# Performance work log

Hardware: AMD Instinct MI355X
Metric: run time of the kernel (lower is better)

## Reference

```python
import jax, jax.numpy as jnp
import numpy as np

N = 50000      # nodes
IN = 256       # in_feat
H = 4          # num_heads
DH = 64        # out_feat // num_heads
R = 6          # number of relations
E = 300000     # edges per relation
NEG_SLOPE = 0.2  # DGL GATConv leaky_relu slope


def setup_inputs() -> dict:
    key = jax.random.key(0)
    ks = jax.random.split(key, 7)
    x = jax.random.normal(ks[0], (N, IN), dtype=jnp.float32)
    W = jax.random.normal(ks[1], (R, IN, H * DH), dtype=jnp.float32) * (1.0 / np.sqrt(IN))
    attn_l = jax.random.normal(ks[2], (R, H, DH), dtype=jnp.float32) * 0.1
    attn_r = jax.random.normal(ks[3], (R, H, DH), dtype=jnp.float32) * 0.1
    bias = jax.random.normal(ks[4], (R, H * DH), dtype=jnp.float32) * 0.01
    src = jax.random.randint(ks[5], (R, E), 0, N, dtype=jnp.int32).astype(jnp.int64)
    dst = jax.random.randint(ks[6], (R, E), 0, N, dtype=jnp.int32).astype(jnp.int64)
    return {"x": x, "W": W, "attn_l": attn_l, "attn_r": attn_r, "bias": bias,
            "src": src, "dst": dst}


def reference(x, W, attn_l, attn_r, bias, src, dst):
    n = x.shape[0]
    r_total, h, dh = attn_l.shape
    out = jnp.zeros((n, h, dh), dtype=x.dtype)
    # small fixed loop over structurally-distinct relations (HeteroGraphConv)
    for r in range(r_total):
        feat = (x @ W[r]).reshape(n, h, dh)            # [N,H,Dh] shared src/dst proj
        el = jnp.sum(feat * attn_l[r], axis=-1)        # [N,H]
        er = jnp.sum(feat * attn_r[r], axis=-1)        # [N,H]
        s, d = src[r], dst[r]
        e = jax.nn.leaky_relu(el[s] + er[d], NEG_SLOPE)  # [E,H]
        # segmented softmax over incoming edges of each dst node
        m = jax.ops.segment_max(e, d, num_segments=n)    # [N,H]
        m = jnp.where(jnp.isfinite(m), m, 0.0)
        a = jnp.exp(e - m[d])                            # [E,H]
        z = jax.ops.segment_sum(a, d, num_segments=n)    # [N,H]
        alpha = a / jnp.maximum(z[d], 1e-9)              # [E,H]
        msg = alpha[:, :, None] * feat[s]                # [E,H,Dh]
        agg = jax.ops.segment_sum(msg, d, num_segments=n)  # [N,H,Dh]
        # GATConv: bias + activation(relu) per relation, HeteroGraphConv sums
        out = out + jax.nn.relu(agg + bias[r].reshape(h, dh))
    hcat = out.reshape(n, h * dh)                        # merge='cat' view
    return jax.nn.relu(hcat)                             # layer-level activation
```

## Files before the change

kernel.cpp:

```cpp
#include <hip/hip_runtime.h>

#define NN 50000
#define MP 50048
#define NH 4
#define NR 6
#define NE 300000
#define HD 256
#define SLOTS 32
#define NB 512
#define BSZ ((NE + NB - 1) / NB)

typedef __attribute__((ext_vector_type(4))) float f32x4;
typedef __attribute__((ext_vector_type(8))) short bf16x8;

__device__ __forceinline__ short f2bf(float f) {
  unsigned u = __float_as_uint(f);
  unsigned r = (u + 0x7FFFu + ((u >> 16) & 1u)) >> 16;
  return (short)r;
}
__device__ __forceinline__ float bf2f_lo(unsigned d) {
  return __uint_as_float(d << 16);
}
__device__ __forceinline__ float bf2f_hi(unsigned d) {
  return __uint_as_float(d & 0xffff0000u);
}

#define GLOAD_LDS16(g, l)                                                     \
  __builtin_amdgcn_global_load_lds(                                           \
      (const __attribute__((address_space(1))) void*)(g),                     \
      (__attribute__((address_space(3))) void*)(l), 16, 0, 0)

__global__ __launch_bounds__(256) void cast_x_kernel(
    const float* __restrict__ x, short* __restrict__ xb, int n4) {
  const int i = blockIdx.x * 256 + threadIdx.x;
  if (i >= n4) return;
  const float4 v = ((const float4*)x)[i];
  short4 o;
  o.x = f2bf(v.x); o.y = f2bf(v.y); o.z = f2bf(v.z); o.w = f2bf(v.w);
  ((short4*)xb)[i] = o;
}

__global__ __launch_bounds__(256) void cast_wt_kernel(
    const float* __restrict__ W, short* __restrict__ wt) {
  __shared__ float ts[32][33];
  const int bx = blockIdx.x;
  const int r = bx >> 6;
  const int tile = bx & 63;
  const int k0 = (tile >> 3) * 32;
  const int n0 = (tile & 7) * 32;
  const int t = threadIdx.x;
  const int col = t & 31;
  const int rr = t >> 5;
#pragma unroll
  for (int p = 0; p < 4; ++p) {
    const int row = p * 8 + rr;
    ts[row][col] = W[(size_t)r * 65536 + (k0 + row) * 256 + n0 + col];
  }
  __syncthreads();
#pragma unroll
  for (int p = 0; p < 4; ++p) {
    const int row = p * 8 + rr;
    wt[(size_t)r * 65536 + (n0 + row) * 256 + k0 + col] = f2bf(ts[col][row]);
  }
}

__global__ __launch_bounds__(256) void wlwr_kernel(
    const float* __restrict__ W, const float* __restrict__ attn_l,
    const float* __restrict__ attn_r, short* __restrict__ wlwr) {
  const int idx = blockIdx.x * 256 + threadIdx.x;
  if (idx >= 128 * 256) return;
  const int k = idx & 255;
  const int n = idx >> 8;
  float v = 0.f;
  if (n < 48) {
    const int r = n >> 3, h = (n >> 1) & 3, side = n & 1;
    const float* a = (side ? attn_r : attn_l) + r * 256 + h * 64;
    const float* wrow = W + (size_t)r * 65536 + (size_t)k * 256 + h * 64;
#pragma unroll 8
    for (int dh = 0; dh < 64; ++dh) v = fmaf(wrow[dh], a[dh], v);
  }
  wlwr[(size_t)n * 256 + k] = f2bf(v);
}

__global__ __launch_bounds__(256) void eler_kernel(
    const short* __restrict__ xb, const short* __restrict__ wlwr,
    float* __restrict__ el_all, float* __restrict__ er_all) {
  __shared__ short As[128 * 64];
  __shared__ short Bs[128 * 64];
  const int t = threadIdx.x;
  const int lane = t & 63;
  const int w = t >> 6;
  const int wm = w & 1, wn = w >> 1;
  const int row0 = blockIdx.x * 128;

  f32x4 acc[4][4];
#pragma unroll
  for (int mi = 0; mi < 4; ++mi)
#pragma unroll
    for (int ni = 0; ni < 4; ++ni) {
      f32x4 z = {0.f, 0.f, 0.f, 0.f};
      acc[mi][ni] = z;
    }

  const short* ag[4];
  const short* bg[4];
  short* la[4];
  short* lb[4];
#pragma unroll
  for (int i = 0; i < 4; ++i) {
    const int c = t + 256 * i;
    const int row = c >> 3;
    const int sslot = (c & 7) ^ (row & 7);
    int ar = row0 + row; if (ar >= NN) ar = NN - 1;
    ag[i] = xb + (size_t)ar * 256 + sslot * 8;
    bg[i] = wlwr + (size_t)row * 256 + sslot * 8;
    la[i] = As + c * 8;
    lb[i] = Bs + c * 8;
  }

  const int ra = lane & 15;
  const int qg = lane >> 4;

  for (int k0 = 0; k0 < 256; k0 += 64) {
#pragma unroll
    for (int i = 0; i < 4; ++i) {
      GLOAD_LDS16(ag[i] + k0, la[i]);
      GLOAD_LDS16(bg[i] + k0, lb[i]);
    }
    __syncthreads();
#pragma unroll
    for (int kk = 0; kk < 2; ++kk) {
      bf16x8 af[4], bfr[4];
#pragma unroll
      for (int mi = 0; mi < 4; ++mi) {
        const int rw = wm * 64 + mi * 16 + ra;
        const int ch = (kk * 4 + qg) ^ (rw & 7);
        af[mi] = *(const bf16x8*)&As[rw * 64 + ch * 8];
      }
#pragma unroll
      for (int ni = 0; ni < 4; ++ni) {
        const int rw = wn * 64 + ni * 16 + ra;
        const int ch = (kk * 4 + qg) ^ (rw & 7);
        bfr[ni] = *(const bf16x8*)&Bs[rw * 64 + ch * 8];
      }
#pragma unroll
      for (int mi = 0; mi < 4; ++mi)
#pragma unroll
        for (int ni = 0; ni < 4; ++ni)
          acc[mi][ni] = __builtin_amdgcn_mfma_f32_16x16x32_bf16(
              af[mi], bfr[ni], acc[mi][ni], 0, 0, 0);
    }
    __syncthreads();
  }

#pragma unroll
  for (int mi = 0; mi < 4; ++mi) {
#pragma unroll
    for (int j = 0; j < 4; ++j) {
      const int row = row0 + wm * 64 + mi * 16 + (lane >> 4) * 4 + j;
      if (row >= NN) continue;
#pragma unroll
      for (int ni = 0; ni < 4; ++ni) {
        const int c = wn * 64 + ni * 16 + ra;
        if (c < 48) {
          const int r = c >> 3, h = (c >> 1) & 3, side = c & 1;
          float* dstp = (side ? er_all : el_all);
          dstp[((size_t)r * NN + row) * NH + h] = acc[mi][ni][j];
        }
      }
    }
  }
}

__global__ __launch_bounds__(256) void gemm_kernel(
    const short* __restrict__ xb,
    const short* __restrict__ wt_all,
    short* __restrict__ featb_all) {
  __shared__ short As[128 * 64];
  __shared__ short Bs[128 * 64];
  const int t = threadIdx.x;
  const int lane = t & 63;
  const int w = t >> 6;
  const int wm = w & 1, wn = w >> 1;
  const int row0 = blockIdx.x * 128;
  const int n0 = blockIdx.y * 128;
  const int r = blockIdx.z;
  const short* wt = wt_all + (size_t)r * 65536;
  short* featb = featb_all + (size_t)r * MP * 256;

  f32x4 acc[4][4];
#pragma unroll
  for (int mi = 0; mi < 4; ++mi)
#pragma unroll
    for (int ni = 0; ni < 4; ++ni) {
      f32x4 z = {0.f, 0.f, 0.f, 0.f};
      acc[mi][ni] = z;
    }

  const short* ag[4];
  const short* bg[4];
  short* la[4];
  short* lb[4];
#pragma unroll
  for (int i = 0; i < 4; ++i) {
    const int c = t + 256 * i;
    const int row = c >> 3;
    const int sslot = (c & 7) ^ (row & 7);
    int ar = row0 + row; if (ar >= NN) ar = NN - 1;
    ag[i] = xb + (size_t)ar * 256 + sslot * 8;
    bg[i] = wt + (size_t)(n0 + row) * 256 + sslot * 8;
    la[i] = As + c * 8;
    lb[i] = Bs + c * 8;
  }

  const int ra = lane & 15;
  const int qg = lane >> 4;

  for (int k0 = 0; k0 < 256; k0 += 64) {
#pragma unroll
    for (int i = 0; i < 4; ++i) {
      GLOAD_LDS16(ag[i] + k0, la[i]);
      GLOAD_LDS16(bg[i] + k0, lb[i]);
    }
    __syncthreads();
#pragma unroll
    for (int kk = 0; kk < 2; ++kk) {
      bf16x8 af[4], bfr[4];
#pragma unroll
      for (int mi = 0; mi < 4; ++mi) {
        const int rw = wm * 64 + mi * 16 + ra;
        const int ch = (kk * 4 + qg) ^ (rw & 7);
        af[mi] = *(const bf16x8*)&As[rw * 64 + ch * 8];
      }
#pragma unroll
      for (int ni = 0; ni < 4; ++ni) {
        const int rw = wn * 64 + ni * 16 + ra;
        const int ch = (kk * 4 + qg) ^ (rw & 7);
        bfr[ni] = *(const bf16x8*)&Bs[rw * 64 + ch * 8];
      }
#pragma unroll
      for (int mi = 0; mi < 4; ++mi)
#pragma unroll
        for (int ni = 0; ni < 4; ++ni)
          acc[mi][ni] = __builtin_amdgcn_mfma_f32_16x16x32_bf16(
              af[mi], bfr[ni], acc[mi][ni], 0, 0, 0);
    }
    __syncthreads();
  }

#pragma unroll
  for (int mi = 0; mi < 4; ++mi) {
#pragma unroll
    for (int j = 0; j < 4; ++j) {
      const int row = row0 + wm * 64 + mi * 16 + (lane >> 4) * 4 + j;
#pragma unroll
      for (int ni = 0; ni < 4; ++ni)
        featb[(size_t)row * 256 + n0 + wn * 64 + ni * 16 + ra] =
            f2bf(acc[mi][ni][j]);
    }
  }
}

__global__ __launch_bounds__(256) void build_kernel(
    const int* __restrict__ src, const int* __restrict__ dst,
    int* __restrict__ deg, unsigned short* __restrict__ slots) {
  const int lo = blockIdx.x * BSZ;
  const int hi = (lo + BSZ < NE) ? lo + BSZ : NE;
  for (int r = 0; r < NR; ++r) {
    for (int i = lo + threadIdx.x; i < hi; i += 256) {
      const int s = src[(size_t)r * NE + i];
      const int d = dst[(size_t)r * NE + i];
      const int g = r * NN + d;
      const int sl = atomicAdd(&deg[g], 1);
      if (sl < SLOTS)
        slots[(size_t)g * SLOTS + sl] = (unsigned short)s;
    }
  }
}

__global__ __launch_bounds__(256) void agg_kernel(
    const short* __restrict__ featb_all, const float* __restrict__ el_all,
    const float* __restrict__ er_all, const int* __restrict__ deg,
    const unsigned short* __restrict__ slots, const float* __restrict__ bias,
    float* __restrict__ out) {
  const int wid = (blockIdx.x * 256 + threadIdx.x) >> 6;
  const int lane = threadIdx.x & 63;
  if (wid >= NN) return;
  const int h = lane >> 4;
  const int c0 = lane * 4;

  float oacc[4] = {0.f, 0.f, 0.f, 0.f};
  const int wid_u = __builtin_amdgcn_readfirstlane(wid);

  const int g_first = (NR - 1) * NN + wid_u;
  const uint4* spf = (const uint4*)(slots + (size_t)g_first * SLOTS);
  uint4 sq0 = spf[0], sq1 = spf[1], sq2 = spf[2], sq3 = spf[3];
  int dgv = deg[g_first];
  float erv = er_all[(size_t)g_first * NH + h];

  for (int r = NR - 1; r >= 0; --r) {
    const int dg0 = __builtin_amdgcn_readfirstlane(dgv);
    const int dg = dg0 > SLOTS ? SLOTS : dg0;
    unsigned sdv[16];
    sdv[0]  = __builtin_amdgcn_readfirstlane(sq0.x);
    sdv[1]  = __builtin_amdgcn_readfirstlane(sq0.y);
    sdv[2]  = __builtin_amdgcn_readfirstlane(sq0.z);
    sdv[3]  = __builtin_amdgcn_readfirstlane(sq0.w);
    sdv[4]  = __builtin_amdgcn_readfirstlane(sq1.x);
    sdv[5]  = __builtin_amdgcn_readfirstlane(sq1.y);
    sdv[6]  = __builtin_amdgcn_readfirstlane(sq1.z);
    sdv[7]  = __builtin_amdgcn_readfirstlane(sq1.w);
    sdv[8]  = __builtin_amdgcn_readfirstlane(sq2.x);
    sdv[9]  = __builtin_amdgcn_readfirstlane(sq2.y);
    sdv[10] = __builtin_amdgcn_readfirstlane(sq2.z);
    sdv[11] = __builtin_amdgcn_readfirstlane(sq2.w);
    sdv[12] = __builtin_amdgcn_readfirstlane(sq3.x);
    sdv[13] = __builtin_amdgcn_readfirstlane(sq3.y);
    sdv[14] = __builtin_amdgcn_readfirstlane(sq3.z);
    sdv[15] = __builtin_amdgcn_readfirstlane(sq3.w);
    const float er_nh = erv;

    if (r > 0) {
      const int g2 = (r - 1) * NN + wid_u;
      const uint4* sp2 = (const uint4*)(slots + (size_t)g2 * SLOTS);
      sq0 = sp2[0]; sq1 = sp2[1]; sq2 = sp2[2]; sq3 = sp2[3];
      dgv = deg[g2];
      erv = er_all[(size_t)g2 * NH + h];
    }

    const float* elr = el_all + (size_t)r * NN * NH;
    const short* fb = featb_all + (size_t)r * MP * 256;

    float z = 0.f;
    float acc[4] = {0.f, 0.f, 0.f, 0.f};

#pragma unroll
    for (int j0 = 0; j0 < SLOTS; j0 += 8) {
      if (j0 >= dg) break;
      float pv[8];
      uint2 rw[8];
#pragma unroll
      for (int k = 0; k < 8; ++k) {
        const int e = j0 + k;
        int s = (int)((e & 1) ? (sdv[e >> 1] >> 16) : (sdv[e >> 1] & 0xffffu));
        const bool v = e < dg;
        s = v ? s : 0;
        rw[k] = *(const uint2*)(fb + (size_t)s * 256 + c0);
        float ev = elr[s * NH + h] + er_nh;
        ev = fmaxf(ev, 0.2f * ev);
        pv[k] = v ? __expf(ev) : 0.f;
      }
#pragma unroll
      for (int k = 0; k < 8; ++k) {
        z += pv[k];
        acc[0] = fmaf(pv[k], bf2f_lo(rw[k].x), acc[0]);
        acc[1] = fmaf(pv[k], bf2f_hi(rw[k].x), acc[1]);
        acc[2] = fmaf(pv[k], bf2f_lo(rw[k].y), acc[2]);
        acc[3] = fmaf(pv[k], bf2f_hi(rw[k].y), acc[3]);
      }
    }

    const float inv = 1.f / fmaxf(z, 1e-9f);
    const float4 bv = *(const float4*)(bias + r * HD + c0);
    oacc[0] += fmaxf(fmaf(acc[0], inv, bv.x), 0.f);
    oacc[1] += fmaxf(fmaf(acc[1], inv, bv.y), 0.f);
    oacc[2] += fmaxf(fmaf(acc[2], inv, bv.z), 0.f);
    oacc[3] += fmaxf(fmaf(acc[3], inv, bv.w), 0.f);
  }

  float4 o4 = {oacc[0], oacc[1], oacc[2], oacc[3]};
  *(float4*)(out + (size_t)wid * 256 + c0) = o4;
}

extern "C" void kernel_launch(void* const* d_in, const int* in_sizes, int n_in,
                              void* d_out, int out_size, void* d_ws,
                              size_t ws_size, hipStream_t stream) {
  const float* x      = (const float*)d_in[0];
  const float* W      = (const float*)d_in[1];
  const float* attn_l = (const float*)d_in[2];
  const float* attn_r = (const float*)d_in[3];
  const float* bias   = (const float*)d_in[4];
  const int*   src    = (const int*)d_in[5];
  const int*   dst    = (const int*)d_in[6];
  float* out = (float*)d_out;

  char* p = (char*)d_ws;
  auto alloc = [&](size_t bytes) {
    char* r = p;
    p += (bytes + 255) & ~(size_t)255;
    return r;
  };
  short* xb    = (short*)alloc((size_t)NN * HD * 2);
  short* wt    = (short*)alloc((size_t)NR * 256 * 256 * 2);
  short* wlwr  = (short*)alloc((size_t)128 * 256 * 2);
  short* featb = (short*)alloc((size_t)NR * MP * 256 * 2);
  float* el    = (float*)alloc((size_t)NR * NN * NH * 4);
  float* er    = (float*)alloc((size_t)NR * NN * NH * 4);
  int*   deg   = (int*)alloc((size_t)NR * NN * 4);
  unsigned short* slots =
      (unsigned short*)alloc((size_t)NR * NN * SLOTS * 2);

  hipMemsetAsync(deg, 0, (size_t)NR * NN * 4, stream);

  cast_x_kernel<<<(NN * HD / 4 + 255) / 256, 256, 0, stream>>>(x, xb,
                                                               NN * HD / 4);
  cast_wt_kernel<<<NR * 64, 256, 0, stream>>>(W, wt);
  wlwr_kernel<<<128, 256, 0, stream>>>(W, attn_l, attn_r, wlwr);
  build_kernel<<<NB, 256, 0, stream>>>(src, dst, deg, slots);
  eler_kernel<<<MP / 128, 256, 0, stream>>>(xb, wlwr, el, er);
  gemm_kernel<<<dim3(MP / 128, 2, NR), 256, 0, stream>>>(xb, wt, featb);
  agg_kernel<<<(NN * 64) / 256, 256, 0, stream>>>(featb, el, er, deg, slots,
                                                  bias, out);
}
```

Baseline: 458.2 us.

## Replace fixed-slot adjacency with compact padded CSR via count, scan, fill

```diff
diff --git a/kernel.cpp b/kernel.cpp
--- a/kernel.cpp
+++ b/kernel.cpp
@@ -7,6 +7,7 @@
 #define NE 300000
 #define HD 256
 #define SLOTS 32
+#define NG (NR * NN)
 #define NB 512
 #define BSZ ((NE + NB - 1) / NB)
 
@@ -261,19 +262,80 @@
   }
 }
 
-__global__ __launch_bounds__(256) void build_kernel(
+
+__global__ __launch_bounds__(256) void count_kernel(
+    const int* __restrict__ dst, int* __restrict__ deg) {
+  const int lo = blockIdx.x * BSZ;
+  const int hi = (lo + BSZ < NE) ? lo + BSZ : NE;
+  for (int r = 0; r < NR; ++r)
+    for (int i = lo + threadIdx.x; i < hi; i += 256)
+      atomicAdd(&deg[r * NN + dst[(size_t)r * NE + i]], 1);
+}
+
+__global__ __launch_bounds__(1024) void scan_kernel(
+    const int* __restrict__ deg, unsigned* __restrict__ off,
+    unsigned* __restrict__ cursor) {
+  __shared__ unsigned wsum[16];
+  __shared__ unsigned carry_s;
+  const int t = threadIdx.x;
+  const int lane = t & 63;
+  const int wv = t >> 6;
+  if (t == 0) carry_s = 0;
+  __syncthreads();
+  for (int base = 0; base < NG; base += 8192) {
+    unsigned v[8];
+    unsigned tsum = 0;
+    const int g0 = base + t * 8;
+#pragma unroll
+    for (int j = 0; j < 8; ++j) {
+      const int g = g0 + j;
+      const unsigned d = (g < NG) ? (unsigned)deg[g] : 0u;
+      v[j] = (d + 7u) & ~7u;
+      tsum += v[j];
+    }
+    unsigned sc = tsum;
+#pragma unroll
+    for (int s = 1; s < 64; s <<= 1) {
+      const unsigned u = __shfl_up(sc, s, 64);
+      if (lane >= s) sc += u;
+    }
+    if (lane == 63) wsum[wv] = sc;
+    __syncthreads();
+    if (wv == 0 && lane < 16) {
+      unsigned ws = wsum[lane];
+#pragma unroll
+      for (int s = 1; s < 16; s <<= 1) {
+        const unsigned u = __shfl_up(ws, s, 64);
+        if (lane >= s) ws += u;
+      }
+      wsum[lane] = ws;
+    }
+    __syncthreads();
+    const unsigned wbase = (wv == 0) ? 0u : wsum[wv - 1];
+    unsigned run = carry_s + wbase + (sc - tsum);
+#pragma unroll
+    for (int j = 0; j < 8; ++j) {
+      const int g = g0 + j;
+      if (g < NG) { off[g] = run; cursor[g] = run; }
+      run += v[j];
+    }
+    __syncthreads();
+    if (t == 0) carry_s += wsum[15];
+    __syncthreads();
+  }
+}
+
+__global__ __launch_bounds__(256) void fill_kernel(
     const int* __restrict__ src, const int* __restrict__ dst,
-    int* __restrict__ deg, unsigned short* __restrict__ slots) {
+    unsigned* __restrict__ cursor, unsigned short* __restrict__ csr) {
   const int lo = blockIdx.x * BSZ;
   const int hi = (lo + BSZ < NE) ? lo + BSZ : NE;
   for (int r = 0; r < NR; ++r) {
     for (int i = lo + threadIdx.x; i < hi; i += 256) {
       const int s = src[(size_t)r * NE + i];
       const int d = dst[(size_t)r * NE + i];
-      const int g = r * NN + d;
-      const int sl = atomicAdd(&deg[g], 1);
-      if (sl < SLOTS)
-        slots[(size_t)g * SLOTS + sl] = (unsigned short)s;
+      const unsigned pos = atomicAdd(&cursor[r * NN + d], 1u);
+      csr[pos] = (unsigned short)s;
     }
   }
 }
@@ -281,8 +343,8 @@
 __global__ __launch_bounds__(256) void agg_kernel(
     const short* __restrict__ featb_all, const float* __restrict__ el_all,
     const float* __restrict__ er_all, const int* __restrict__ deg,
-    const unsigned short* __restrict__ slots, const float* __restrict__ bias,
-    float* __restrict__ out) {
+    const unsigned* __restrict__ off, const unsigned short* __restrict__ csr,
+    const float* __restrict__ bias, float* __restrict__ out) {
   const int wid = (blockIdx.x * 256 + threadIdx.x) >> 6;
   const int lane = threadIdx.x & 63;
   if (wid >= NN) return;
@@ -293,7 +355,7 @@
   const int wid_u = __builtin_amdgcn_readfirstlane(wid);
 
   const int g_first = (NR - 1) * NN + wid_u;
-  const uint4* spf = (const uint4*)(slots + (size_t)g_first * SLOTS);
+  const uint4* spf = (const uint4*)(csr + off[g_first]);
   uint4 sq0 = spf[0], sq1 = spf[1], sq2 = spf[2], sq3 = spf[3];
   int dgv = deg[g_first];
   float erv = er_all[(size_t)g_first * NH + h];
@@ -322,7 +384,7 @@
 
     if (r > 0) {
       const int g2 = (r - 1) * NN + wid_u;
-      const uint4* sp2 = (const uint4*)(slots + (size_t)g2 * SLOTS);
+      const uint4* sp2 = (const uint4*)(csr + off[g2]);
       sq0 = sp2[0]; sq1 = sp2[1]; sq2 = sp2[2]; sq3 = sp2[3];
       dgv = deg[g2];
       erv = er_all[(size_t)g2 * NH + h];
@@ -396,19 +458,23 @@
   short* featb = (short*)alloc((size_t)NR * MP * 256 * 2);
   float* el    = (float*)alloc((size_t)NR * NN * NH * 4);
   float* er    = (float*)alloc((size_t)NR * NN * NH * 4);
-  int*   deg   = (int*)alloc((size_t)NR * NN * 4);
-  unsigned short* slots =
-      (unsigned short*)alloc((size_t)NR * NN * SLOTS * 2);
-
-  hipMemsetAsync(deg, 0, (size_t)NR * NN * 4, stream);
+  int*   deg   = (int*)alloc((size_t)NG * 4);
+  unsigned* off    = (unsigned*)alloc((size_t)NG * 4);
+  unsigned* cursor = (unsigned*)alloc((size_t)NG * 4);
+  unsigned short* csr =
+      (unsigned short*)alloc(((size_t)NR * NE + (size_t)NG * 8 + 64) * 2);
+
+  hipMemsetAsync(deg, 0, (size_t)NG * 4, stream);
 
   cast_x_kernel<<<(NN * HD / 4 + 255) / 256, 256, 0, stream>>>(x, xb,
                                                                NN * HD / 4);
   cast_wt_kernel<<<NR * 64, 256, 0, stream>>>(W, wt);
   wlwr_kernel<<<128, 256, 0, stream>>>(W, attn_l, attn_r, wlwr);
-  build_kernel<<<NB, 256, 0, stream>>>(src, dst, deg, slots);
+  count_kernel<<<NB, 256, 0, stream>>>(dst, deg);
+  scan_kernel<<<1, 1024, 0, stream>>>(deg, off, cursor);
+  fill_kernel<<<NB, 256, 0, stream>>>(src, dst, cursor, csr);
   eler_kernel<<<MP / 128, 256, 0, stream>>>(xb, wlwr, el, er);
   gemm_kernel<<<dim3(MP / 128, 2, NR), 256, 0, stream>>>(xb, wt, featb);
-  agg_kernel<<<(NN * 64) / 256, 256, 0, stream>>>(featb, el, er, deg, slots,
-                                                  bias, out);
-}
+  agg_kernel<<<(NN * 64) / 256, 256, 0, stream>>>(featb, el, er, deg, off,
+                                                  csr, bias, out);
+}
```

Result: slower. 912.5 us (+99.1%).

## Keep full-K x tile resident in LDS and loop relations inside GEMM block

Applied to the files above, without the earlier changes.

```diff
diff --git a/kernel.cpp b/kernel.cpp
--- a/kernel.cpp
+++ b/kernel.cpp
@@ -176,7 +176,7 @@
     const short* __restrict__ xb,
     const short* __restrict__ wt_all,
     short* __restrict__ featb_all) {
-  __shared__ short As[128 * 64];
+  __shared__ short As[128 * 256];
   __shared__ short Bs[128 * 64];
   const int t = threadIdx.x;
   const int lane = t & 63;
@@ -184,79 +184,82 @@
   const int wm = w & 1, wn = w >> 1;
   const int row0 = blockIdx.x * 128;
   const int n0 = blockIdx.y * 128;
-  const int r = blockIdx.z;
-  const short* wt = wt_all + (size_t)r * 65536;
-  short* featb = featb_all + (size_t)r * MP * 256;
-
-  f32x4 acc[4][4];
-#pragma unroll
-  for (int mi = 0; mi < 4; ++mi)
-#pragma unroll
-    for (int ni = 0; ni < 4; ++ni) {
-      f32x4 z = {0.f, 0.f, 0.f, 0.f};
-      acc[mi][ni] = z;
-    }
-
-  const short* ag[4];
-  const short* bg[4];
-  short* la[4];
-  short* lb[4];
+
+#pragma unroll
+  for (int i = 0; i < 16; ++i) {
+    const int c = t + 256 * i;
+    const int row = c >> 5;
+    const int slot = (c & 31) ^ (row & 31);
+    int ar = row0 + row; if (ar >= NN) ar = NN - 1;
+    GLOAD_LDS16(xb + (size_t)ar * 256 + slot * 8, As + c * 8);
+  }
+
+  size_t bsrc[4];
+  short* bdst[4];
 #pragma unroll
   for (int i = 0; i < 4; ++i) {
     const int c = t + 256 * i;
     const int row = c >> 3;
-    const int sslot = (c & 7) ^ (row & 7);
-    int ar = row0 + row; if (ar >= NN) ar = NN - 1;
-    ag[i] = xb + (size_t)ar * 256 + sslot * 8;
-    bg[i] = wt + (size_t)(n0 + row) * 256 + sslot * 8;
-    la[i] = As + c * 8;
-    lb[i] = Bs + c * 8;
+    const int slot = (c & 7) ^ (row & 7);
+    bsrc[i] = (size_t)(n0 + row) * 256 + slot * 8;
+    bdst[i] = Bs + c * 8;
   }
 
   const int ra = lane & 15;
   const int qg = lane >> 4;
 
-  for (int k0 = 0; k0 < 256; k0 += 64) {
-#pragma unroll
-    for (int i = 0; i < 4; ++i) {
-      GLOAD_LDS16(ag[i] + k0, la[i]);
-      GLOAD_LDS16(bg[i] + k0, lb[i]);
-    }
-    __syncthreads();
-#pragma unroll
-    for (int kk = 0; kk < 2; ++kk) {
-      bf16x8 af[4], bfr[4];
-#pragma unroll
-      for (int mi = 0; mi < 4; ++mi) {
-        const int rw = wm * 64 + mi * 16 + ra;
-        const int ch = (kk * 4 + qg) ^ (rw & 7);
-        af[mi] = *(const bf16x8*)&As[rw * 64 + ch * 8];
-      }
+  for (int r = 0; r < NR; ++r) {
+    const short* wtr = wt_all + (size_t)r * 65536;
+    f32x4 acc[4][4];
+#pragma unroll
+    for (int mi = 0; mi < 4; ++mi)
 #pragma unroll
       for (int ni = 0; ni < 4; ++ni) {
-        const int rw = wn * 64 + ni * 16 + ra;
-        const int ch = (kk * 4 + qg) ^ (rw & 7);
-        bfr[ni] = *(const bf16x8*)&Bs[rw * 64 + ch * 8];
-      }
-#pragma unroll
-      for (int mi = 0; mi < 4; ++mi)
+        f32x4 z = {0.f, 0.f, 0.f, 0.f};
+        acc[mi][ni] = z;
+      }
+
+    for (int s = 0; s < 4; ++s) {
+#pragma unroll
+      for (int i = 0; i < 4; ++i)
+        GLOAD_LDS16(wtr + bsrc[i] + s * 64, bdst[i]);
+      __syncthreads();
+#pragma unroll
+      for (int kk = 0; kk < 2; ++kk) {
+        bf16x8 af[4], bfr[4];
+#pragma unroll
+        for (int mi = 0; mi < 4; ++mi) {
+          const int rw = wm * 64 + mi * 16 + ra;
+          const int sl = (s * 8 + kk * 4 + qg) ^ (rw & 31);
+          af[mi] = *(const bf16x8*)&As[rw * 256 + sl * 8];
+        }
+#pragma unroll
+        for (int ni = 0; ni < 4; ++ni) {
+          const int rwb = wn * 64 + ni * 16 + ra;
+          const int ch = (kk * 4 + qg) ^ (rwb & 7);
+          bfr[ni] = *(const bf16x8*)&Bs[rwb * 64 + ch * 8];
+        }
+#pragma unroll
+        for (int mi = 0; mi < 4; ++mi)
+#pragma unroll
+          for (int ni = 0; ni < 4; ++ni)
+            acc[mi][ni] = __builtin_amdgcn_mfma_f32_16x16x32_bf16(
+                af[mi], bfr[ni], acc[mi][ni], 0, 0, 0);
+      }
+      __syncthreads();
+    }
+
+    short* featb = featb_all + (size_t)r * MP * 256;
+#pragma unroll
+    for (int mi = 0; mi < 4; ++mi) {
+#pragma unroll
+      for (int j = 0; j < 4; ++j) {
+        const int row = row0 + wm * 64 + mi * 16 + qg * 4 + j;
 #pragma unroll
         for (int ni = 0; ni < 4; ++ni)
-          acc[mi][ni] = __builtin_amdgcn_mfma_f32_16x16x32_bf16(
-              af[mi], bfr[ni], acc[mi][ni], 0, 0, 0);
-    }
-    __syncthreads();
-  }
-
-#pragma unroll
-  for (int mi = 0; mi < 4; ++mi) {
-#pragma unroll
-    for (int j = 0; j < 4; ++j) {
-      const int row = row0 + wm * 64 + mi * 16 + (lane >> 4) * 4 + j;
-#pragma unroll
-      for (int ni = 0; ni < 4; ++ni)
-        featb[(size_t)row * 256 + n0 + wn * 64 + ni * 16 + ra] =
-            f2bf(acc[mi][ni][j]);
+          featb[(size_t)row * 256 + n0 + wn * 64 + ni * 16 + ra] =
+              f2bf(acc[mi][ni][j]);
+      }
     }
   }
 }
@@ -408,7 +411,7 @@
   wlwr_kernel<<<128, 256, 0, stream>>>(W, attn_l, attn_r, wlwr);
   build_kernel<<<NB, 256, 0, stream>>>(src, dst, deg, slots);
   eler_kernel<<<MP / 128, 256, 0, stream>>>(xb, wlwr, el, er);
-  gemm_kernel<<<dim3(MP / 128, 2, NR), 256, 0, stream>>>(xb, wt, featb);
+  gemm_kernel<<<dim3(MP / 128, 2), 256, 0, stream>>>(xb, wt, featb);
   agg_kernel<<<(NN * 64) / 256, 256, 0, stream>>>(featb, el, er, deg, slots,
                                                   bias, out);
 }
```

New measurement: 497.4 us. 1.09x slower.
